# Kernel optimization log

Hardware: AMD Instinct MI355X
Metric: run time of the kernel (lower is better)

The kernel has to match this reference:

```python
import jax, jax.numpy as jnp
import numpy as np

B, S, D, H = 2, 2048, 1024, 16
HD = D // H                      # 64
NUM_ROPE_DIMS = 2
NF = HD // (2 * NUM_ROPE_DIMS)   # 16 freqs per rope dim -> total HD//2
FFN_H = 4 * D


def householder_matrix(vs):
    """Product of Householder reflections: Q = prod_i (I - 2 v_i v_i^T / ||v_i||^2)."""
    dim = vs.shape[-1]
    def step(Q, v):
        v = v[:, None]
        Q = Q - (2.0 / (jnp.sum(v * v) + 1e-8)) * (v @ (v.T @ Q))
        return Q, None
    Q, _ = jax.lax.scan(step, jnp.eye(dim, dtype=vs.dtype), vs)
    return Q


def rmsnorm(x):
    # torch.nn.RMSNorm(eps=None) uses dtype eps, no affine
    return x * jax.lax.rsqrt(jnp.mean(x * x, axis=-1, keepdims=True) + jnp.finfo(x.dtype).eps)


def setup_inputs() -> dict:
    key = jax.random.key(0)
    ks = jax.random.split(key, 8)
    x = jax.random.normal(ks[0], (B, S, D), jnp.float32)
    mask = jnp.tril(jnp.ones((S, S), dtype=bool))          # causal block mask
    qkv_w = jax.random.normal(ks[1], (3 * D, D), jnp.float32) * 0.02
    out_w = jax.random.normal(ks[2], (D, D), jnp.float32) * 0.02
    gate_w = jax.random.normal(ks[3], (D, D), jnp.float32) * 0.02
    gate_b = jnp.zeros((D,), jnp.float32)
    w12 = jax.random.normal(ks[4], (2 * FFN_H, D), jnp.float32) * 0.02
    w3 = jax.random.normal(ks[5], (D, FFN_H), jnp.float32) * 0.02
    hh_vs = jax.random.normal(ks[6], (HD // 2, HD), jnp.float32) * 0.02
    inv_freq = 1.0 / (10000.0 ** (jnp.arange(NF, dtype=jnp.float32) / NF))
    pos = jnp.arange(S, dtype=jnp.float32)
    rope_pos = jnp.stack([pos, pos], axis=-1)              # [S, num_rope_dims]
    return dict(x=x, mask=mask, qkv_w=qkv_w, out_w=out_w, gate_w=gate_w,
                gate_b=gate_b, w12=w12, w3=w3, hh_vs=hh_vs,
                inv_freq=inv_freq, rope_pos=rope_pos)


def reference(x, mask, qkv_w, out_w, gate_w, gate_b, w12, w3, hh_vs, inv_freq, rope_pos):
    Bs, Ss, Ds = x.shape
    resid = x
    xn = rmsnorm(x)
    qkv = xn @ qkv_w.T                                      # [B,S,3D]
    q, k, v = jnp.split(qkv, 3, axis=-1)
    q = q.reshape(Bs, Ss, H, HD).transpose(0, 2, 1, 3)      # [B,H,S,HD]
    k = k.reshape(Bs, Ss, H, HD).transpose(0, 2, 1, 3)
    v = v.reshape(Bs, Ss, H, HD).transpose(0, 2, 1, 3)

    # RnRoPE: rotate into canonical basis, apply RoPE, rotate back
    Q = householder_matrix(hh_vs)                           # [HD,HD]
    q = q @ Q.T
    k = k @ Q.T
    # geo_state.scale = 1.0
    full = jnp.einsum('sd,f->sdf', rope_pos, inv_freq).reshape(Ss, -1)  # [S, HD//2]
    half = HD // 2
    full = full[:, :half]
    emb = jnp.concatenate([full, full], axis=-1)            # [S, HD]
    cos, sin = jnp.cos(emb), jnp.sin(emb)

    def rot(t):
        t1, t2 = jnp.split(t, 2, axis=-1)
        return t * cos + jnp.concatenate([-t2, t1], axis=-1) * sin

    q = rot(q) @ Q
    k = rot(k) @ Q

    # block-masked attention (flex_attention default scale = 1/sqrt(HD))
    scores = jnp.einsum('bhsd,bhtd->bhst', q, k) / jnp.sqrt(jnp.asarray(HD, x.dtype))
    scores = jnp.where(mask, scores, -jnp.inf)
    attn = jax.nn.softmax(scores, axis=-1)
    o = jnp.einsum('bhst,bhtd->bhsd', attn, v)
    o = o.transpose(0, 2, 1, 3).reshape(Bs, Ss, Ds)
    o = o @ out_w.T
    gate = jax.nn.sigmoid(o @ gate_w.T + gate_b)
    x = resid + o * gate

    # SwiGLU FFN
    resid2 = x
    xn2 = rmsnorm(x)
    x12 = xn2 @ w12.T
    x1, x2 = jnp.split(x12, 2, axis=-1)
    ffn = (jax.nn.silu(x1) * x2) @ w3.T
    return resid2 + ffn
```

## Files before the change

kernel.cpp:

```cpp
#include <hip/hip_runtime.h>
#include <hip/hip_bf16.h>
#include <math.h>

constexpr int Bc = 2, Sc = 2048, Dc = 1024, Hc = 16, HDc = 64;
constexpr int D3 = 3 * Dc;

typedef __bf16 bf16x8 __attribute__((ext_vector_type(8)));
typedef float f32x4 __attribute__((ext_vector_type(4)));

__device__ __forceinline__ void gll16(const void* g, void* l) {
  __builtin_amdgcn_global_load_lds((const __attribute__((address_space(1))) unsigned int*)g,
                                   (__attribute__((address_space(3))) unsigned int*)l,
                                   16, 0, 0);
}

__device__ __forceinline__ unsigned short f2bf(float v) {
  __hip_bfloat16 h = __float2bfloat16(v);
  return *(unsigned short*)&h;
}
__device__ __forceinline__ float b2f(unsigned short u) {
  unsigned v = ((unsigned)u) << 16;
  return __uint_as_float(v);
}

#define SBAR() asm volatile("s_barrier" ::: "memory")

__global__ __launch_bounds__(256) void f2b_kernel(const float* __restrict__ in,
                                                  unsigned short* __restrict__ out) {
  int i = blockIdx.x * 256 + threadIdx.x;
  float4 v = ((const float4*)in)[i];
  ushort4 o;
  o.x = f2bf(v.x); o.y = f2bf(v.y); o.z = f2bf(v.z); o.w = f2bf(v.w);
  ((ushort4*)out)[i] = o;
}

__global__ __launch_bounds__(256) void w12i_kernel(const float* __restrict__ in,
                                                   unsigned short* __restrict__ out) {
  int r = blockIdx.x;
  int g = r >> 5, u = r & 31;
  int src = ((u < 16) ? 0 : 4096) + g * 16 + (u & 15);
  float4 v = ((const float4*)(in + (size_t)src * 1024))[threadIdx.x];
  ushort4 o;
  o.x = f2bf(v.x); o.y = f2bf(v.y); o.z = f2bf(v.z); o.w = f2bf(v.w);
  ((ushort4*)(out + (size_t)r * 1024))[threadIdx.x] = o;
}

__global__ __launch_bounds__(256) void rmsnorm_bf16_kernel(const float* __restrict__ in,
                                                           unsigned short* __restrict__ out) {
  int row = blockIdx.x;
  const float4* x4 = (const float4*)(in + (size_t)row * Dc);
  float4 v = x4[threadIdx.x];
  float s = v.x * v.x + v.y * v.y + v.z * v.z + v.w * v.w;
#pragma unroll
  for (int off = 1; off < 64; off <<= 1) s += __shfl_xor(s, off);
  __shared__ float wsum[4];
  if ((threadIdx.x & 63) == 0) wsum[threadIdx.x >> 6] = s;
  __syncthreads();
  float tot = wsum[0] + wsum[1] + wsum[2] + wsum[3];
  float r = rsqrtf(tot * (1.0f / Dc) + 1.1920928955078125e-07f);
  ushort4 o;
  o.x = f2bf(v.x * r); o.y = f2bf(v.y * r); o.z = f2bf(v.z * r); o.w = f2bf(v.w * r);
  ((ushort4*)(out + (size_t)row * Dc))[threadIdx.x] = o;
}

__global__ __launch_bounds__(64) void hh_kernel(const float* __restrict__ vs,
                                                float* __restrict__ Qout) {
  __shared__ float Qm[64][65];
  __shared__ float vsh[64];
  int t = threadIdx.x;
  for (int i = 0; i < 64; ++i) Qm[i][t] = (i == t) ? 1.0f : 0.0f;
  for (int it = 0; it < 32; ++it) {
    __syncthreads();
    vsh[t] = vs[it * 64 + t];
    __syncthreads();
    float nv = 0.0f;
    for (int i = 0; i < 64; ++i) nv += vsh[i] * vsh[i];
    float c = 2.0f / (nv + 1e-8f);
    float wj = 0.0f;
    for (int i = 0; i < 64; ++i) wj += vsh[i] * Qm[i][t];
    for (int i = 0; i < 64; ++i) Qm[i][t] -= c * vsh[i] * wj;
  }
  __syncthreads();
  for (int i = 0; i < 64; ++i) Qout[i * 64 + t] = Qm[i][t];
}

__global__ __launch_bounds__(256) void wqk_kernel(const float* __restrict__ W,
                                                  const float* __restrict__ Qm,
                                                  unsigned short* __restrict__ out) {
  int n = blockIdx.x;
  int r = n & 63;
  int base = n & ~63;
  int t = threadIdx.x;
  float a0 = 0, a1 = 0, a2 = 0, a3 = 0;
  const float4* Wp = (const float4*)(W + (size_t)base * 1024) + t;
#pragma unroll 8
  for (int e = 0; e < 64; ++e) {
    float q = Qm[r * 64 + e];
    float4 wv = Wp[(size_t)e * 256];
    a0 += q * wv.x; a1 += q * wv.y; a2 += q * wv.z; a3 += q * wv.w;
  }
  float sc = (n < 1024) ? 0.18033688f : 1.0f;
  ushort4 o;
  o.x = f2bf(a0 * sc); o.y = f2bf(a1 * sc); o.z = f2bf(a2 * sc); o.w = f2bf(a3 * sc);
  ((ushort4*)(out + (size_t)n * 1024))[t] = o;
}

__global__ __launch_bounds__(256) void rtab_kernel(const float* __restrict__ rope_pos,
                                                   const float* __restrict__ inv_freq,
                                                   float2* __restrict__ tab) {
  int id = blockIdx.x * 256 + threadIdx.x;
  int s = id >> 5, d = id & 31;
  float pos = rope_pos[s * 2 + (d >> 4)];
  float emb = pos * inv_freq[d & 15];
  tab[id] = make_float2(cosf(emb), sinf(emb));
}

__global__ __launch_bounds__(256) void rope_kernel(const unsigned short* __restrict__ qkv,
                                                   const float2* __restrict__ tab,
                                                   unsigned short* __restrict__ qb,
                                                   unsigned short* __restrict__ kb) {
  int t = threadIdx.x;
  int gid = blockIdx.x * 64 + (t >> 2);
  int sub = t & 3;
  int h = gid & 15;
  int which = (gid >> 4) & 1;
  int tok = gid >> 5;
  int s = tok & (Sc - 1), b = tok >> 11;
  const unsigned short* src = qkv + (size_t)tok * D3 + which * Dc + h * 64 + sub * 8;
  uint4 lov = *(const uint4*)src;
  uint4 hiv = *(const uint4*)(src + 32);
  const unsigned short* lp = (const unsigned short*)&lov;
  const unsigned short* hp = (const unsigned short*)&hiv;
  unsigned short olo[8], ohi[8];
  const float2* tp = tab + s * 32 + sub * 8;
#pragma unroll
  for (int i = 0; i < 8; ++i) {
    float2 cs = tp[i];
    float lo = b2f(lp[i]), hi = b2f(hp[i]);
    olo[i] = f2bf(lo * cs.x - hi * cs.y);
    ohi[i] = f2bf(hi * cs.x + lo * cs.y);
  }
  unsigned short* dst = (which ? kb : qb) + ((size_t)((b * Hc + h) * Sc + s)) * 64 + sub * 8;
  *(uint4*)dst = *(uint4*)olo;
  *(uint4*)(dst + 32) = *(uint4*)ohi;
}

__global__ __launch_bounds__(256) void vt_kernel(const unsigned short* __restrict__ qkv,
                                                 unsigned short* __restrict__ vtb) {
  __shared__ unsigned short tile[64 * 72];
  int st = blockIdx.x;
  int bh = blockIdx.y;
  int b = bh >> 4, h = bh & 15;
  int t = threadIdx.x;
  int srow = t >> 2, c16 = (t & 3) * 16;
  const unsigned short* src =
      qkv + (size_t)(b * Sc + st * 64 + srow) * D3 + 2 * Dc + h * 64 + c16;
  uint4 a0 = *(const uint4*)src;
  uint4 a1 = *(const uint4*)(src + 8);
  *(uint4*)(tile + srow * 72 + c16) = a0;
  *(uint4*)(tile + srow * 72 + c16 + 8) = a1;
  __syncthreads();
  int d = t >> 2, sch = (t & 3) * 16;
  unsigned short tmp[16];
#pragma unroll
  for (int i = 0; i < 16; ++i) tmp[i] = tile[(sch + i) * 72 + d];
  unsigned short* dst = vtb + ((size_t)(bh * 64 + d)) * Sc + st * 64 + sch;
  *(uint4*)dst = *(uint4*)tmp;
  *(uint4*)(dst + 8) = *(uint4*)(tmp + 8);
}

template <int MODE>
__global__ __launch_bounds__(512, 1) void mgemm8p(const unsigned short* __restrict__ A,
                                                  const unsigned short* __restrict__ B,
                                                  unsigned short* __restrict__ C,
                                                  int M, int N, int K) {
  __shared__ unsigned short lds[65536];
  const int t = threadIdx.x;
  const int lane = t & 63;
  const int wave = t >> 6;
  const int wr = wave >> 2, wc = wave & 3;
  const int l15 = lane & 15, l4 = lane >> 4;
  const int gx = gridDim.x;
  const int nwg = gx * gridDim.y;
  const int id = blockIdx.y * gx + blockIdx.x;
  const int swz = (id & 7) * (nwg >> 3) + (id >> 3);
  const int m0 = (swz / gx) * 256;
  const int n0 = (swz % gx) * 256;
  const int NT = K >> 6;
  const int sko = (((t & 3) ^ ((t >> 3) & 3)) * 8);
  const unsigned short* ag0 = A + (size_t)(m0 + (t >> 2)) * K + sko;
  const unsigned short* ag1 = ag0 + (size_t)128 * K;
  const unsigned short* bg0 = B + (size_t)(n0 + (t >> 2)) * K + sko;
  const unsigned short* bg1 = bg0 + (size_t)128 * K;
  const int t8 = t * 8;
  const int ks = (l4 ^ ((l15 >> 1) & 3)) * 8;
  gll16(ag0, lds + t8);
  gll16(ag1, lds + 4096 + t8);
  gll16(bg0, lds + 32768 + t8);
  gll16(bg1, lds + 32768 + 4096 + t8);
  gll16(ag0 + 32, lds + 8192 + t8);
  gll16(ag1 + 32, lds + 8192 + 4096 + t8);
  gll16(bg0 + 32, lds + 32768 + 8192 + t8);
  gll16(bg1 + 32, lds + 32768 + 8192 + 4096 + t8);
  asm volatile("s_waitcnt vmcnt(4)" ::: "memory");
  SBAR();
  f32x4 acc[8][4] = {};
  for (int kt = 0; kt < NT; ++kt) {
    const int cur = (kt & 1) << 14;
    const int nxt = cur ^ 16384;
    const int kof = ((kt + 1 < NT) ? (kt + 1) : kt) << 6;
    const unsigned short* Ap = lds + cur;
    const unsigned short* Bp = lds + 32768 + cur;
    bf16x8 a[8], b0, b1;
#pragma unroll
    for (int i = 0; i < 8; ++i)
      a[i] = *(const bf16x8*)(Ap + (wr * 128 + i * 16 + l15) * 32 + ks);
    b0 = *(const bf16x8*)(Bp + (wc * 64 + l15) * 32 + ks);
    b1 = *(const bf16x8*)(Bp + (wc * 64 + 16 + l15) * 32 + ks);
    gll16(ag0 + kof, lds + nxt + t8);
    gll16(ag1 + kof, lds + nxt + 4096 + t8);
    SBAR();
    __builtin_amdgcn_s_setprio(1);
#pragma unroll
    for (int i = 0; i < 8; ++i) {
      acc[i][0] = __builtin_amdgcn_mfma_f32_16x16x32_bf16(a[i], b0, acc[i][0], 0, 0, 0);
      acc[i][1] = __builtin_amdgcn_mfma_f32_16x16x32_bf16(a[i], b1, acc[i][1], 0, 0, 0);
    }
    __builtin_amdgcn_s_setprio(0);
    SBAR();
    b0 = *(const bf16x8*)(Bp + (wc * 64 + 32 + l15) * 32 + ks);
    b1 = *(const bf16x8*)(Bp + (wc * 64 + 48 + l15) * 32 + ks);
    gll16(bg0 + kof, lds + 32768 + nxt + t8);
    gll16(bg1 + kof, lds + 32768 + nxt + 4096 + t8);
    asm volatile("s_waitcnt vmcnt(4)" ::: "memory");
    SBAR();
    __builtin_amdgcn_s_setprio(1);
#pragma unroll
    for (int i = 0; i < 8; ++i) {
      acc[i][2] = __builtin_amdgcn_mfma_f32_16x16x32_bf16(a[i], b0, acc[i][2], 0, 0, 0);
      acc[i][3] = __builtin_amdgcn_mfma_f32_16x16x32_bf16(a[i], b1, acc[i][3], 0, 0, 0);
    }
    __builtin_amdgcn_s_setprio(0);
    SBAR();
#pragma unroll
    for (int i = 0; i < 8; ++i)
      a[i] = *(const bf16x8*)(Ap + 8192 + (wr * 128 + i * 16 + l15) * 32 + ks);
    b0 = *(const bf16x8*)(Bp + 8192 + (wc * 64 + l15) * 32 + ks);
    b1 = *(const bf16x8*)(Bp + 8192 + (wc * 64 + 16 + l15) * 32 + ks);
    gll16(ag0 + kof + 32, lds + nxt + 8192 + t8);
    gll16(ag1 + kof + 32, lds + nxt + 8192 + 4096 + t8);
    SBAR();
    __builtin_amdgcn_s_setprio(1);
#pragma unroll
    for (int i = 0; i < 8; ++i) {
      acc[i][0] = __builtin_amdgcn_mfma_f32_16x16x32_bf16(a[i], b0, acc[i][0], 0, 0, 0);
      acc[i][1] = __builtin_amdgcn_mfma_f32_16x16x32_bf16(a[i], b1, acc[i][1], 0, 0, 0);
    }
    __builtin_amdgcn_s_setprio(0);
    SBAR();
    b0 = *(const bf16x8*)(Bp + 8192 + (wc * 64 + 32 + l15) * 32 + ks);
    b1 = *(const bf16x8*)(Bp + 8192 + (wc * 64 + 48 + l15) * 32 + ks);
    gll16(bg0 + kof + 32, lds + 32768 + nxt + 8192 + t8);
    gll16(bg1 + kof + 32, lds + 32768 + nxt + 8192 + 4096 + t8);
    asm volatile("s_waitcnt vmcnt(4)" ::: "memory");
    SBAR();
    __builtin_amdgcn_s_setprio(1);
#pragma unroll
    for (int i = 0; i < 8; ++i) {
      acc[i][2] = __builtin_amdgcn_mfma_f32_16x16x32_bf16(a[i], b0, acc[i][2], 0, 0, 0);
      acc[i][3] = __builtin_amdgcn_mfma_f32_16x16x32_bf16(a[i], b1, acc[i][3], 0, 0, 0);
    }
    __builtin_amdgcn_s_setprio(0);
    SBAR();
  }
  asm volatile("s_waitcnt vmcnt(0)" ::: "memory");
  const int r0 = m0 + wr * 128 + l4 * 4;
  if (MODE == 0) {
    const int c0 = n0 + wc * 64 + l15;
#pragma unroll
    for (int i = 0; i < 8; ++i)
#pragma unroll
      for (int j = 0; j < 4; ++j)
#pragma unroll
        for (int r = 0; r < 4; ++r)
          C[(size_t)(r0 + i * 16 + r) * N + c0 + j * 16] = f2bf(acc[i][j][r]);
  } else {
    const int nc = N >> 1;
    const int c0 = (n0 >> 1) + wc * 32 + l15;
#pragma unroll
    for (int i = 0; i < 8; ++i)
#pragma unroll
      for (int p = 0; p < 2; ++p)
#pragma unroll
        for (int r = 0; r < 4; ++r) {
          float v = acc[i][2 * p][r];
          float sv = v / (1.0f + __expf(-v));
          C[(size_t)(r0 + i * 16 + r) * nc + c0 + p * 16] = f2bf(sv * acc[i][2 * p + 1][r]);
        }
  }
}

template <int MODE>
__global__ __launch_bounds__(256, 3) void mgemm64(const unsigned short* __restrict__ A,
                                                  const unsigned short* __restrict__ W,
                                                  const float* __restrict__ R,
                                                  const float* __restrict__ R2,
                                                  const float* __restrict__ bias,
                                                  void* __restrict__ Cout,
                                                  void* __restrict__ Cout2,
                                                  int M, int N, int K) {
  __shared__ unsigned short As[2][2][2048];
  __shared__ unsigned short Bs[2][2][4096];
  const int t = threadIdx.x;
  const int lane = t & 63;
  const int wave = t >> 6;
  const int wr = wave >> 1, wc = wave & 1;
  const int gx = gridDim.x;
  const int nwg = gx * gridDim.y;
  const int id = blockIdx.y * gx + blockIdx.x;
  const int swz = (id & 7) * (nwg >> 3) + (id >> 3);
  const int m0 = (swz / gx) * 64, n0 = (swz % gx) * 128;
  f32x4 acc[2][4] = {};
  const int srow = t >> 2;
  const int sch = (((t & 3) ^ ((t >> 3) & 3)) * 8);
  const unsigned short* Ag = A + (size_t)(m0 + srow) * K + sch;
  const unsigned short* Wg = W + (size_t)(n0 + srow) * K + sch;
  const size_t rstep = (size_t)64 * K;
  const int frow = lane & 15;
  const int l4 = lane >> 4;
  const int fk = (l4 ^ ((frow >> 1) & 3)) * 8;
  const int t8 = t * 8;
  gll16(Ag, As[0][0] + t8);
  gll16(Ag + 32, As[0][1] + t8);
  gll16(Wg, Bs[0][0] + t8);
  gll16(Wg + rstep, Bs[0][0] + 2048 + t8);
  gll16(Wg + 32, Bs[0][1] + t8);
  gll16(Wg + rstep + 32, Bs[0][1] + 2048 + t8);
  for (int k0 = 0; k0 < K; k0 += 64) {
    const int cur = (k0 >> 6) & 1;
    const int kn = (k0 + 64 < K) ? (k0 + 64) : k0;
    gll16(Ag + kn, As[cur ^ 1][0] + t8);
    gll16(Ag + kn + 32, As[cur ^ 1][1] + t8);
    gll16(Wg + kn, Bs[cur ^ 1][0] + t8);
    gll16(Wg + kn + rstep, Bs[cur ^ 1][0] + 2048 + t8);
    gll16(Wg + kn + 32, Bs[cur ^ 1][1] + t8);
    gll16(Wg + kn + rstep + 32, Bs[cur ^ 1][1] + 2048 + t8);
    asm volatile("s_waitcnt vmcnt(6)" ::: "memory");
    SBAR();
#pragma unroll
    for (int kh = 0; kh < 2; ++kh) {
      bf16x8 af[2], bq[4];
#pragma unroll
      for (int i = 0; i < 2; ++i)
        af[i] = *(const bf16x8*)(As[cur][kh] + (wr * 32 + i * 16 + frow) * 32 + fk);
#pragma unroll
      for (int j = 0; j < 4; ++j)
        bq[j] = *(const bf16x8*)(Bs[cur][kh] + (wc * 64 + j * 16 + frow) * 32 + fk);
      __builtin_amdgcn_s_setprio(1);
#pragma unroll
      for (int i = 0; i < 2; ++i)
#pragma unroll
        for (int j = 0; j < 4; ++j)
          acc[i][j] = __builtin_amdgcn_mfma_f32_16x16x32_bf16(af[i], bq[j], acc[i][j], 0, 0, 0);
      __builtin_amdgcn_s_setprio(0);
    }
    SBAR();
  }
  asm volatile("s_waitcnt vmcnt(0)" ::: "memory");
  const int crow = wr * 32 + (lane >> 4) * 4;
  const int ccol = wc * 64 + (lane & 15);
#pragma unroll
  for (int i = 0; i < 2; ++i) {
#pragma unroll
    for (int j = 0; j < 4; ++j) {
#pragma unroll
      for (int r = 0; r < 4; ++r) {
        int row = m0 + crow + i * 16 + r;
        int col = n0 + ccol + j * 16;
        float v = acc[i][j][r];
        size_t off = (size_t)row * N + col;
        if (MODE == 2) {
          ((float*)Cout)[off] = v + R[off];
        } else if (MODE == 4) {
          ((float*)Cout)[off] = v;
          ((unsigned short*)Cout2)[off] = f2bf(v);
        } else {
          float g = v + bias[col];
          float sg = 1.0f / (1.0f + __expf(-g));
          ((float*)Cout)[off] = R[off] + R2[off] * sg;
        }
      }
    }
  }
}

__global__ __launch_bounds__(256, 3) void mattn(const unsigned short* __restrict__ qb,
                                                const unsigned short* __restrict__ kb,
                                                const unsigned short* __restrict__ vtb,
                                                float* __restrict__ opart,
                                                float* __restrict__ lpart) {
  __shared__ unsigned short Qs[8192];
  __shared__ unsigned short Ks[2][4096];
  __shared__ unsigned short Vts[4096];
  __shared__ unsigned short Ps[4 * 16 * 72];
  const int bidx = 39 - blockIdx.x;
  int qt, s;
  if (bidx < 4)       { qt = bidx;                  s = 0; }
  else if (bidx < 12) { qt = 4 + ((bidx - 4) >> 1); s = (bidx - 4) & 1; }
  else if (bidx < 24) { int u = bidx - 12; int q3 = u / 3; qt = 8 + q3; s = u - 3 * q3; }
  else                { qt = 12 + ((bidx - 24) >> 2); s = (bidx - 24) & 3; }
  const int nt = 2 * qt + 2;
  const int kt0 = s * 8;
  const int kt1 = (kt0 + 8 < nt) ? kt0 + 8 : nt;
  const int bh = blockIdx.y;
  const int t = threadIdx.x, lane = t & 63, w = t >> 6;
  const int l15 = lane & 15, l4 = lane >> 4;
  const unsigned short* qbase = qb + ((size_t)bh * Sc + qt * 128) * 64;
  const unsigned short* kbase = kb + (size_t)bh * Sc * 64;
  const unsigned short* vbase = vtb + (size_t)bh * 64 * Sc;
#pragma unroll
  for (int i = 0; i < 4; ++i) {
    int idx = t + i * 256;
    int r = idx >> 3;
    int cg = (idx & 7) ^ (r & 7);
    gll16(qbase + (size_t)r * 64 + cg * 8, Qs + idx * 8);
  }
  const int sr = t >> 3;
  const int scg = (t & 7) ^ (sr & 7);
  gll16(vbase + (size_t)sr * Sc + kt0 * 64 + scg * 8, Vts + t * 8);
  gll16(vbase + (size_t)(sr + 32) * Sc + kt0 * 64 + scg * 8, Vts + 2048 + t * 8);
  gll16(kbase + (size_t)(kt0 * 64 + sr) * 64 + scg * 8, Ks[0] + t * 8);
  gll16(kbase + (size_t)(kt0 * 64 + sr + 32) * 64 + scg * 8, Ks[0] + 2048 + t * 8);
  bf16x8 qf[2][2];
  f32x4 oacc[2][4] = {};
  float lrow[2][4] = {};
  unsigned short* pw = Ps + w * 16 * 72;
  for (int kt = kt0; kt < kt1; ++kt) {
    const int cur = kt & 1;
    if (kt > kt0) {
      gll16(vbase + (size_t)sr * Sc + kt * 64 + scg * 8, Vts + t * 8);
      gll16(vbase + (size_t)(sr + 32) * Sc + kt * 64 + scg * 8, Vts + 2048 + t * 8);
    }
    const int ktn = (kt + 1 < kt1) ? kt + 1 : kt;
    gll16(kbase + (size_t)(ktn * 64 + sr) * 64 + scg * 8, Ks[cur ^ 1] + t * 8);
    gll16(kbase + (size_t)(ktn * 64 + sr + 32) * 64 + scg * 8, Ks[cur ^ 1] + 2048 + t * 8);
    if (kt == kt0) {
      asm volatile("s_waitcnt vmcnt(2)" ::: "memory");
    } else {
      asm volatile("s_waitcnt vmcnt(4)" ::: "memory");
    }
    SBAR();
    if (kt == kt0) {
#pragma unroll
      for (int ch = 0; ch < 2; ++ch) {
        int qrow = ch * 64 + w * 16 + l15;
#pragma unroll
        for (int kc = 0; kc < 2; ++kc)
          qf[ch][kc] = *(const bf16x8*)(Qs + qrow * 64 + (((kc * 4 + l4) ^ (l15 & 7)) * 8));
      }
    }
    const bool actA = (kt <= 2 * qt);
    f32x4 sc[2][4] = {};
#pragma unroll
    for (int kc = 0; kc < 2; ++kc) {
      bf16x8 kf[4];
#pragma unroll
      for (int j = 0; j < 4; ++j)
        kf[j] = *(const bf16x8*)(Ks[cur] + (j * 16 + l15) * 64 + (((kc * 4 + l4) ^ (l15 & 7)) * 8));
      __builtin_amdgcn_s_setprio(1);
      if (actA) {
#pragma unroll
        for (int j = 0; j < 4; ++j)
          sc[0][j] = __builtin_amdgcn_mfma_f32_16x16x32_bf16(qf[0][kc], kf[j], sc[0][j], 0, 0, 0);
      }
#pragma unroll
      for (int j = 0; j < 4; ++j)
        sc[1][j] = __builtin_amdgcn_mfma_f32_16x16x32_bf16(qf[1][kc], kf[j], sc[1][j], 0, 0, 0);
      __builtin_amdgcn_s_setprio(0);
    }
    const int rl = w * 16 + l4 * 4;
    if (kt == 2 * qt) {
#pragma unroll
      for (int j = 0; j < 4; ++j)
#pragma unroll
        for (int r = 0; r < 4; ++r)
          if (j * 16 + l15 > rl + r) sc[0][j][r] = -INFINITY;
    }
    if (kt == 2 * qt + 1) {
#pragma unroll
      for (int j = 0; j < 4; ++j)
#pragma unroll
        for (int r = 0; r < 4; ++r)
          if (j * 16 + l15 > rl + r) sc[1][j][r] = -INFINITY;
    }
    asm volatile("s_waitcnt vmcnt(2)" ::: "memory");
    SBAR();
    bf16x8 vf[2][4];
#pragma unroll
    for (int kc = 0; kc < 2; ++kc)
#pragma unroll
      for (int j = 0; j < 4; ++j)
        vf[kc][j] = *(const bf16x8*)(Vts + (j * 16 + l15) * 64 + (((kc * 4 + l4) ^ (l15 & 7)) * 8));
#pragma unroll
    for (int ch = 0; ch < 2; ++ch) {
      if (ch == 0 && !actA) continue;
#pragma unroll
      for (int j = 0; j < 4; ++j)
#pragma unroll
        for (int r = 0; r < 4; ++r) {
          float p = exp2f(sc[ch][j][r]);
          lrow[ch][r] += p;
          pw[(l4 * 4 + r) * 72 + j * 16 + l15] = f2bf(p);
        }
      __asm__ __volatile__("s_waitcnt lgkmcnt(0)" ::: "memory");
      __builtin_amdgcn_s_setprio(1);
#pragma unroll
      for (int kc = 0; kc < 2; ++kc) {
        bf16x8 pf = *(const bf16x8*)(pw + l15 * 72 + kc * 32 + l4 * 8);
#pragma unroll
        for (int j = 0; j < 4; ++j)
          oacc[ch][j] = __builtin_amdgcn_mfma_f32_16x16x32_bf16(pf, vf[kc][j], oacc[ch][j], 0, 0, 0);
      }
      __builtin_amdgcn_s_setprio(0);
    }
    SBAR();
  }
  asm volatile("s_waitcnt vmcnt(0)" ::: "memory");
  float* opr = opart + ((size_t)(bh * 40 + bidx) * 128) * 64;
  float* lpr = lpart + (bh * 40 + bidx) * 128;
#pragma unroll
  for (int ch = 0; ch < 2; ++ch) {
#pragma unroll
    for (int r = 0; r < 4; ++r) {
      float sum = lrow[ch][r];
      sum += __shfl_xor(sum, 1);
      sum += __shfl_xor(sum, 2);
      sum += __shfl_xor(sum, 4);
      sum += __shfl_xor(sum, 8);
      const int row = ch * 64 + w * 16 + l4 * 4 + r;
      if (l15 == 0) lpr[row] = sum;
#pragma unroll
      for (int j = 0; j < 4; ++j)
        opr[(size_t)row * 64 + j * 16 + l15] = oacc[ch][j][r];
    }
  }
}

__global__ __launch_bounds__(256) void acomb(const float* __restrict__ Op,
                                             const float* __restrict__ lp,
                                             unsigned short* __restrict__ out) {
  const int qt = blockIdx.x, bh = blockIdx.y;
  const int b = bh >> 4, h = bh & 15;
  const int ns = (qt >> 2) + 1;
  const int base = (qt < 4) ? qt
                 : (qt < 8) ? 4 + 2 * (qt - 4)
                 : (qt < 12) ? 12 + 3 * (qt - 8)
                 : 24 + 4 * (qt - 12);
  const int t = threadIdx.x;
  const int row = t >> 1, d0 = (t & 1) * 32;
  float l = 0.0f;
  float acc[32] = {};
  for (int s = 0; s < ns; ++s) {
    const int pidx = bh * 40 + base + s;
    l += lp[pidx * 128 + row];
    const float4* src = (const float4*)(Op + ((size_t)pidx * 128 + row) * 64 + d0);
#pragma unroll
    for (int i = 0; i < 8; ++i) {
      float4 v = src[i];
      acc[i * 4 + 0] += v.x; acc[i * 4 + 1] += v.y;
      acc[i * 4 + 2] += v.z; acc[i * 4 + 3] += v.w;
    }
  }
  const float inv = 1.0f / l;
  unsigned short* dst = out + ((size_t)(b * Sc + qt * 128 + row)) * Dc + h * 64 + d0;
#pragma unroll
  for (int i = 0; i < 8; ++i) {
    ushort4 o;
    o.x = f2bf(acc[i * 4 + 0] * inv); o.y = f2bf(acc[i * 4 + 1] * inv);
    o.z = f2bf(acc[i * 4 + 2] * inv); o.w = f2bf(acc[i * 4 + 3] * inv);
    ((ushort4*)dst)[i] = o;
  }
}

extern "C" void kernel_launch(void* const* d_in, const int* in_sizes, int n_in,
                              void* d_out, int out_size, void* d_ws, size_t ws_size,
                              hipStream_t stream) {
  const float* x        = (const float*)d_in[0];
  const float* qkv_w    = (const float*)d_in[2];
  const float* out_w    = (const float*)d_in[3];
  const float* gate_w   = (const float*)d_in[4];
  const float* gate_b   = (const float*)d_in[5];
  const float* w12      = (const float*)d_in[6];
  const float* w3       = (const float*)d_in[7];
  const float* hh_vs    = (const float*)d_in[8];
  const float* inv_freq = (const float*)d_in[9];
  const float* rope_pos = (const float*)d_in[10];
  char* ws = (char*)d_ws;
  unsigned short* woutb  = (unsigned short*)(ws + 0);
  float2*         rtab   = (float2*)(ws + 2097152);
  unsigned short* wqkvb  = (unsigned short*)(ws + 4194304);
  unsigned short* attnb  = (unsigned short*)(ws + 4194304);
  float*          lpart  = (float*)(ws + 12582912);
  float*          xmid   = (float*)(ws + 0);
  unsigned short* slotB  = (unsigned short*)(ws + 16777216);
  float*          opart  = (float*)(ws + 16777216);
  float*          oproj  = (float*)(ws + 25165824);
  unsigned short* w12b   = (unsigned short*)(ws + 25165824);
  unsigned short* w3b    = (unsigned short*)(ws + 41943040);
  unsigned short* qkvb   = (unsigned short*)(ws + 58720256);
  unsigned short* wgateb = (unsigned short*)(ws + 58720256);
  unsigned short* hbufb  = (unsigned short*)(ws + 58720256);
  unsigned short* qb     = (unsigned short*)(ws + 83886080);
  unsigned short* oprojb = (unsigned short*)(ws + 83886080);
  unsigned short* kb     = (unsigned short*)(ws + 92274688);
  unsigned short* vtb    = (unsigned short*)(ws + 100663296);
  float*          Qb     = (float*)(ws + 109051904);
  float* outp = (float*)d_out;

  hh_kernel<<<1, 64, 0, stream>>>(hh_vs, Qb);
  rtab_kernel<<<256, 256, 0, stream>>>(rope_pos, inv_freq, rtab);
  wqk_kernel<<<2048, 256, 0, stream>>>(qkv_w, Qb, wqkvb);
  f2b_kernel<<<1024, 256, 0, stream>>>(qkv_w + 2048 * 1024,
                                       wqkvb + 2048 * 1024);
  f2b_kernel<<<1024, 256, 0, stream>>>(out_w, woutb);
  rmsnorm_bf16_kernel<<<4096, 256, 0, stream>>>(x, slotB);
  mgemm8p<0><<<dim3(12, 16), 512, 0, stream>>>(slotB, wqkvb, qkvb, 4096, 3072, 1024);
  rope_kernel<<<2048, 256, 0, stream>>>(qkvb, rtab, qb, kb);
  vt_kernel<<<dim3(32, 32), 256, 0, stream>>>(qkvb, vtb);
  f2b_kernel<<<1024, 256, 0, stream>>>(gate_w, wgateb);
  mattn<<<dim3(40, 32), 256, 0, stream>>>(qb, kb, vtb, opart, lpart);
  acomb<<<dim3(16, 32), 256, 0, stream>>>(opart, lpart, attnb);
  mgemm64<4><<<dim3(8, 64), 256, 0, stream>>>(attnb, woutb, nullptr, nullptr, nullptr,
                                              oproj, oprojb, 4096, 1024, 1024);
  mgemm64<5><<<dim3(8, 64), 256, 0, stream>>>(oprojb, wgateb, x, oproj, gate_b,
                                              xmid, nullptr, 4096, 1024, 1024);
  w12i_kernel<<<8192, 256, 0, stream>>>(w12, w12b);
  f2b_kernel<<<4096, 256, 0, stream>>>(w3, w3b);
  rmsnorm_bf16_kernel<<<4096, 256, 0, stream>>>(xmid, slotB);
  mgemm8p<1><<<dim3(32, 16), 512, 0, stream>>>(slotB, w12b, hbufb, 4096, 8192, 1024);
  mgemm64<2><<<dim3(8, 64), 256, 0, stream>>>(hbufb, w3b, xmid, nullptr, nullptr,
                                              outp, nullptr, 4096, 1024, 4096);
}
```

Measured before the change: 508.1 us.

## Double-buffer V tiles and load Q fragments directly into registers

The attention kernel no longer stages Q through shared memory: each lane loads its Q fragments straight from global memory into registers. V tiles are now double-buffered like K, so the next V tile is prefetched alongside the next K tile, and the second barrier/wait per iteration is removed. This aims to overlap V loads with compute and cut LDS usage and a synchronisation point, at the cost of an extra 8KB V buffer and uncoalesced direct Q global reads. Correctness of the single remaining barrier depends on the Ks/Vts buffer reuse ordering across iterations.

```diff
diff --git a/kernel.cpp b/kernel.cpp
--- a/kernel.cpp
+++ b/kernel.cpp
@@ -399,9 +399,8 @@
                                                 const unsigned short* __restrict__ vtb,
                                                 float* __restrict__ opart,
                                                 float* __restrict__ lpart) {
-  __shared__ unsigned short Qs[8192];
   __shared__ unsigned short Ks[2][4096];
-  __shared__ unsigned short Vts[4096];
+  __shared__ unsigned short Vts[2][4096];
   __shared__ unsigned short Ps[4 * 16 * 72];
   const int bidx = 39 - blockIdx.x;
   int qt, s;
@@ -418,47 +417,31 @@
   const unsigned short* qbase = qb + ((size_t)bh * Sc + qt * 128) * 64;
   const unsigned short* kbase = kb + (size_t)bh * Sc * 64;
   const unsigned short* vbase = vtb + (size_t)bh * 64 * Sc;
-#pragma unroll
-  for (int i = 0; i < 4; ++i) {
-    int idx = t + i * 256;
-    int r = idx >> 3;
-    int cg = (idx & 7) ^ (r & 7);
-    gll16(qbase + (size_t)r * 64 + cg * 8, Qs + idx * 8);
-  }
+  bf16x8 qf[2][2];
+#pragma unroll
+  for (int ch = 0; ch < 2; ++ch)
+#pragma unroll
+    for (int kc = 0; kc < 2; ++kc)
+      qf[ch][kc] = *(const bf16x8*)(qbase + (size_t)(ch * 64 + w * 16 + l15) * 64 +
+                                    (kc * 4 + l4) * 8);
   const int sr = t >> 3;
   const int scg = (t & 7) ^ (sr & 7);
-  gll16(vbase + (size_t)sr * Sc + kt0 * 64 + scg * 8, Vts + t * 8);
-  gll16(vbase + (size_t)(sr + 32) * Sc + kt0 * 64 + scg * 8, Vts + 2048 + t * 8);
   gll16(kbase + (size_t)(kt0 * 64 + sr) * 64 + scg * 8, Ks[0] + t * 8);
   gll16(kbase + (size_t)(kt0 * 64 + sr + 32) * 64 + scg * 8, Ks[0] + 2048 + t * 8);
-  bf16x8 qf[2][2];
+  gll16(vbase + (size_t)sr * Sc + kt0 * 64 + scg * 8, Vts[0] + t * 8);
+  gll16(vbase + (size_t)(sr + 32) * Sc + kt0 * 64 + scg * 8, Vts[0] + 2048 + t * 8);
   f32x4 oacc[2][4] = {};
   float lrow[2][4] = {};
   unsigned short* pw = Ps + w * 16 * 72;
   for (int kt = kt0; kt < kt1; ++kt) {
-    const int cur = kt & 1;
-    if (kt > kt0) {
-      gll16(vbase + (size_t)sr * Sc + kt * 64 + scg * 8, Vts + t * 8);
-      gll16(vbase + (size_t)(sr + 32) * Sc + kt * 64 + scg * 8, Vts + 2048 + t * 8);
-    }
+    const int cur = (kt - kt0) & 1;
     const int ktn = (kt + 1 < kt1) ? kt + 1 : kt;
     gll16(kbase + (size_t)(ktn * 64 + sr) * 64 + scg * 8, Ks[cur ^ 1] + t * 8);
     gll16(kbase + (size_t)(ktn * 64 + sr + 32) * 64 + scg * 8, Ks[cur ^ 1] + 2048 + t * 8);
-    if (kt == kt0) {
-      asm volatile("s_waitcnt vmcnt(2)" ::: "memory");
-    } else {
-      asm volatile("s_waitcnt vmcnt(4)" ::: "memory");
-    }
-    SBAR();
-    if (kt == kt0) {
-#pragma unroll
-      for (int ch = 0; ch < 2; ++ch) {
-        int qrow = ch * 64 + w * 16 + l15;
-#pragma unroll
-        for (int kc = 0; kc < 2; ++kc)
-          qf[ch][kc] = *(const bf16x8*)(Qs + qrow * 64 + (((kc * 4 + l4) ^ (l15 & 7)) * 8));
-      }
-    }
+    gll16(vbase + (size_t)sr * Sc + ktn * 64 + scg * 8, Vts[cur ^ 1] + t * 8);
+    gll16(vbase + (size_t)(sr + 32) * Sc + ktn * 64 + scg * 8, Vts[cur ^ 1] + 2048 + t * 8);
+    asm volatile("s_waitcnt vmcnt(4)" ::: "memory");
+    SBAR();
     const bool actA = (kt <= 2 * qt);
     f32x4 sc[2][4] = {};
 #pragma unroll
@@ -493,14 +476,12 @@
         for (int r = 0; r < 4; ++r)
           if (j * 16 + l15 > rl + r) sc[1][j][r] = -INFINITY;
     }
-    asm volatile("s_waitcnt vmcnt(2)" ::: "memory");
-    SBAR();
     bf16x8 vf[2][4];
 #pragma unroll
     for (int kc = 0; kc < 2; ++kc)
 #pragma unroll
       for (int j = 0; j < 4; ++j)
-        vf[kc][j] = *(const bf16x8*)(Vts + (j * 16 + l15) * 64 + (((kc * 4 + l4) ^ (l15 & 7)) * 8));
+        vf[kc][j] = *(const bf16x8*)(Vts[cur] + (j * 16 + l15) * 64 + (((kc * 4 + l4) ^ (l15 & 7)) * 8));
 #pragma unroll
     for (int ch = 0; ch < 2; ++ch) {
       if (ch == 0 && !actA) continue;
```

Measured after the change: 513.5 us. About the same (+1.1%).
